# Kernel tuning notes

Measured on AMD Instinct MI355X. Metric: run time of the kernel, lower is better.

Reference implementation:

```python
import jax, jax.numpy as jnp
import numpy as np

SHIFT = 1  # module picks random +-1 at init; fixed deterministically to +1


def setup_inputs() -> dict:
    key = jax.random.key(0)
    k1, k2, k3 = jax.random.split(key, 3)
    x = jax.random.normal(k1, (128, 128, 56, 56), dtype=jnp.float32)
    w0 = jax.random.normal(k2, (2, 3, 3, 32), dtype=jnp.float32)
    w1 = jax.random.normal(k3, (64, 4), dtype=jnp.float32)
    return {"x": x, "w0": w0, "w1": w1}


def _unfold3(t, axis):
    # F.unfold with kernel (3,1), padding (1,0) along `axis` (length 56):
    # zero-pad by 1 on each side, then stack the 3 shifted windows as a new
    # axis placed just BEFORE `axis` (matching torch's C*kh channel ordering
    # after the reshapes in the original module).
    pad = [(0, 0)] * t.ndim
    pad[axis] = (1, 1)
    p = jnp.pad(t, pad)
    slices = []
    for a in range(3):
        idx = [slice(None)] * t.ndim
        idx[axis] = slice(a, a + 56)
        slices.append(p[tuple(idx)])
    return jnp.stack(slices, axis=axis)


def reference(x, w0, w1):
    # x: (128,128,56,56) -> (k=128, j=64, m=2, n=56, l=56)
    t3 = x.reshape(128, 64, 2, 56, 56)
    # channel mix: contract j=64 against w1 (64,4) -> (b, m=2, n=56, l=56, i=4)
    t4 = jnp.einsum('kjmnl,ji->kmnli', t3, w1)
    # first unfold over l (axis 3): (b, 2, 56, kA=3, l=56, i=4)
    u1 = _unfold3(t4, axis=3)
    # second unfold over l again (now axis 4), padding applied to u1 (which
    # already contains zeros from the first padding) -> (b,2,56,kA,kB,l,i)
    u2 = _unfold3(u1, axis=4)
    # torch permute (0,1,2,5,4,3,6): (b, 2, 56, l, kB, kA, i)
    t5 = jnp.transpose(u2, (0, 1, 2, 5, 4, 3, 6))
    # conv-like contraction with w0 (l=2, i=3, k=3, j=32) -> (b,56,56,4,32)
    t6 = jnp.einsum('mlonikp,likj->monpj', t5, w0)
    # (b,56,56,32,4) -> (b,56,56,128), roll along H, -> NCHW
    t7 = jnp.transpose(t6, (0, 1, 2, 4, 3)).reshape(128, 56, 56, 128)
    t7 = jnp.roll(t7, SHIFT, axis=1)
    return jnp.transpose(t7, (0, 3, 1, 2))
```

## Files before the change

kernel.cpp:

```cpp
#include <hip/hip_runtime.h>

namespace {
constexpr int CH = 128, HH = 56, WW = 56;
constexpr int R  = 2;
constexpr int LP = 60;

__global__ __launch_bounds__(256, 6) void fused_conv_kernel(
    const float* __restrict__ x,
    const float* __restrict__ w0,
    const float* __restrict__ w1,
    float* __restrict__ out)
{
    __shared__ float t4s[R][2][4][LP];
    __shared__ float w0s[2 * 3 * 3 * 32];

    const int tid = threadIdx.x;
    const int b   = blockIdx.x / (HH / R);
    const int hg  = blockIdx.x - b * (HH / R);
    const int h0  = hg * R;

    for (int t = tid; t < 576; t += 256) w0s[t] = w0[t];

    if (tid < R * 32) {
        int e = tid;
        const int r = e >> 5; e &= 31;
        const int m = e >> 4; e &= 15;
        const int i = e >> 2;
        const int p = e & 3;
        t4s[r][m][i][(p < 2) ? p : (56 + p)] = 0.f;
    }

    if (tid < R * 112) {
        int e = tid;
        const int r = e / 112; e -= r * 112;
        const int m = e / 56;
        const int l = e - m * 56;
        const float*  xp  = x + (((size_t)b * CH + m) * HH + (h0 + r)) * WW + l;
        const float4* w1v = (const float4*)w1;
        float a0 = 0.f, a1 = 0.f, a2 = 0.f, a3 = 0.f;
        #pragma unroll 8
        for (int j = 0; j < 64; ++j) {
            const float  xv = xp[(size_t)j * (2 * HH * WW)];
            const float4 wv = w1v[j];
            a0 = fmaf(xv, wv.x, a0);
            a1 = fmaf(xv, wv.y, a1);
            a2 = fmaf(xv, wv.z, a2);
            a3 = fmaf(xv, wv.w, a3);
        }
        t4s[r][m][0][2 + l] = a0;
        t4s[r][m][1][2 + l] = a1;
        t4s[r][m][2][2 + l] = a2;
        t4s[r][m][3][2 + l] = a3;
    }
    __syncthreads();

    #pragma unroll 2
    for (int it = 0; it < R * 7; ++it) {
        const int t  = it * 256 + tid;
        const int r  = t / 1792;
        const int tt = t - r * 1792;
        const int c  = tt / 14;
        const int q  = tt - c * 14;
        const int l0 = q * 4;
        const int j  = c >> 2;
        const int i  = c & 3;

        const float* tp0 = &t4s[r][0][i][l0];
        const float* tp1 = &t4s[r][1][i][l0];
        const float4 p0a = *(const float4*)(tp0);
        const float4 p0b = *(const float4*)(tp0 + 4);
        const float4 p1a = *(const float4*)(tp1);
        const float4 p1b = *(const float4*)(tp1 + 4);
        const float v0[8] = {p0a.x, p0a.y, p0a.z, p0a.w, p0b.x, p0b.y, p0b.z, p0b.w};
        const float v1[8] = {p1a.x, p1a.y, p1a.z, p1a.w, p1b.x, p1b.y, p1b.z, p1b.w};

        float acc0 = 0.f, acc1 = 0.f, acc2 = 0.f, acc3 = 0.f;
        #pragma unroll
        for (int m = 0; m < 2; ++m) {
            #pragma unroll
            for (int kB = 0; kB < 3; ++kB) {
                #pragma unroll
                for (int kA = 0; kA < 3; ++kA) {
                    const float wv = w0s[((m * 3 + kB) * 3 + kA) * 32 + j];
                    const int dd = kA + kB;
                    acc0 = fmaf(m ? v1[dd]     : v0[dd],     wv, acc0);
                    acc1 = fmaf(m ? v1[dd + 1] : v0[dd + 1], wv, acc1);
                    acc2 = fmaf(m ? v1[dd + 2] : v0[dd + 2], wv, acc2);
                    acc3 = fmaf(m ? v1[dd + 3] : v0[dd + 3], wv, acc3);
                }
            }
        }

        if (l0 == 0) {
            #pragma unroll
            for (int m = 0; m < 2; ++m)
                acc0 -= t4s[r][m][i][2] * w0s[((m * 3 + 0) * 3 + 2) * 32 + j];
        }
        if (l0 == 52) {
            #pragma unroll
            for (int m = 0; m < 2; ++m)
                acc3 -= t4s[r][m][i][57] * w0s[((m * 3 + 2) * 3 + 0) * 32 + j];
        }

        const int h_out = (h0 + r + 1) % HH;
        float* orow = out + (((size_t)b * CH + c) * HH + h_out) * WW + l0;
        *(float4*)orow = make_float4(acc0, acc1, acc2, acc3);
    }
}
}

extern "C" void kernel_launch(void* const* d_in, const int* in_sizes, int n_in,
                              void* d_out, int out_size, void* d_ws, size_t ws_size,
                              hipStream_t stream) {
    const float* x  = (const float*)d_in[0];
    const float* w0 = (const float*)d_in[1];
    const float* w1 = (const float*)d_in[2];
    float* out = (float*)d_out;
    fused_conv_kernel<<<dim3(128 * (HH / R)), dim3(256), 0, stream>>>(x, w0, w1, out);
}
```

Before: 121.9 us.

## Vectorize channel-mix loads with float4 and split j-reduction across lanes

The channel-mix stage now gives each thread four consecutive l positions and a quarter of the 64 input channels. It issues all 16 float4 global loads up front for more memory-level parallelism, then reduces partial sums across the four lanes with xor shuffles. Each lane writes one of the four outputs to shared memory as float2 stores. Launch bounds drop to 4 blocks per SM to leave room for the extra registers the 16 float4 loads need, at the cost of occupancy.

```diff
diff --git a/kernel.cpp b/kernel.cpp
--- a/kernel.cpp
+++ b/kernel.cpp
@@ -5,7 +5,7 @@
 constexpr int R  = 2;
 constexpr int LP = 60;
 
-__global__ __launch_bounds__(256, 6) void fused_conv_kernel(
+__global__ __launch_bounds__(256, 4) void fused_conv_kernel(
     const float* __restrict__ x,
     const float* __restrict__ w0,
     const float* __restrict__ w1,
@@ -30,27 +30,47 @@
         t4s[r][m][i][(p < 2) ? p : (56 + p)] = 0.f;
     }
 
-    if (tid < R * 112) {
+    if (tid < 224) {
         int e = tid;
-        const int r = e / 112; e -= r * 112;
-        const int m = e / 56;
-        const int l = e - m * 56;
-        const float*  xp  = x + (((size_t)b * CH + m) * HH + (h0 + r)) * WW + l;
+        const int js = e & 3;  e >>= 2;
+        const int lq = e % 14; e /= 14;
+        const int m  = e & 1;
+        const int r  = e >> 1;
+
+        const float* xp = x + (((size_t)b * CH + 2 * (js * 16) + m) * HH + (h0 + r)) * WW + lq * 4;
+        const size_t cstride = (size_t)2 * HH * WW;
+
+        float4 xv[16];
+        #pragma unroll
+        for (int jj = 0; jj < 16; ++jj)
+            xv[jj] = *reinterpret_cast<const float4*>(xp + (size_t)jj * cstride);
+
+        float4 acc[4] = {};
         const float4* w1v = (const float4*)w1;
-        float a0 = 0.f, a1 = 0.f, a2 = 0.f, a3 = 0.f;
-        #pragma unroll 8
-        for (int j = 0; j < 64; ++j) {
-            const float  xv = xp[(size_t)j * (2 * HH * WW)];
-            const float4 wv = w1v[j];
-            a0 = fmaf(xv, wv.x, a0);
-            a1 = fmaf(xv, wv.y, a1);
-            a2 = fmaf(xv, wv.z, a2);
-            a3 = fmaf(xv, wv.w, a3);
+        #pragma unroll
+        for (int jj = 0; jj < 16; ++jj) {
+            const float4 wv = w1v[js * 16 + jj];
+            #pragma unroll
+            for (int i = 0; i < 4; ++i) {
+                const float wvi = (i == 0) ? wv.x : (i == 1) ? wv.y : (i == 2) ? wv.z : wv.w;
+                acc[i].x = fmaf(xv[jj].x, wvi, acc[i].x);
+                acc[i].y = fmaf(xv[jj].y, wvi, acc[i].y);
+                acc[i].z = fmaf(xv[jj].z, wvi, acc[i].z);
+                acc[i].w = fmaf(xv[jj].w, wvi, acc[i].w);
+            }
         }
-        t4s[r][m][0][2 + l] = a0;
-        t4s[r][m][1][2 + l] = a1;
-        t4s[r][m][2][2 + l] = a2;
-        t4s[r][m][3][2 + l] = a3;
+
+        #pragma unroll
+        for (int i = 0; i < 4; ++i) {
+            acc[i].x += __shfl_xor(acc[i].x, 1); acc[i].x += __shfl_xor(acc[i].x, 2);
+            acc[i].y += __shfl_xor(acc[i].y, 1); acc[i].y += __shfl_xor(acc[i].y, 2);
+            acc[i].z += __shfl_xor(acc[i].z, 1); acc[i].z += __shfl_xor(acc[i].z, 2);
+            acc[i].w += __shfl_xor(acc[i].w, 1); acc[i].w += __shfl_xor(acc[i].w, 2);
+        }
+
+        const float4 my = (js == 0) ? acc[0] : (js == 1) ? acc[1] : (js == 2) ? acc[2] : acc[3];
+        *reinterpret_cast<float2*>(&t4s[r][m][js][2 + 4 * lq])     = make_float2(my.x, my.y);
+        *reinterpret_cast<float2*>(&t4s[r][m][js][2 + 4 * lq + 2]) = make_float2(my.z, my.w);
     }
     __syncthreads();
 
```

Result: slower. 141.5 us (+16.0%).
